# Optimization experiments

Measured on AMD Instinct MI355X. Metric: run time of the kernel, lower is better.

## Reference

```python
import jax, jax.numpy as jnp
import numpy as np

DIM, HEADS, DHEAD = 256, 8, 64
HID = HEADS * DHEAD


def _elu1(x):
    # F.elu(x) + 1 == exp(x) for x<0, x+1 for x>=0
    return jnp.where(x > 0, x + 1.0, jnp.exp(x))


def setup_inputs() -> dict:
    key = jax.random.key(0)
    ks = jax.random.split(key, 6)
    B, H, W = 8, 64, 64
    x = jax.random.normal(ks[0], (B, DIM, H, W), dtype=jnp.float32)
    contact_map = jax.random.uniform(ks[1], (B, 1, H, W), dtype=jnp.float32)
    s_qkv = 1.0 / np.sqrt(DIM)
    Wqkv = jax.random.normal(ks[2], (3 * HID, DIM), dtype=jnp.float32) * s_qkv
    s_out = 1.0 / np.sqrt(HID)
    Wout = jax.random.normal(ks[3], (DIM, HID), dtype=jnp.float32) * s_out
    bout = jax.random.normal(ks[4], (DIM,), dtype=jnp.float32) * 0.01
    contact_scale = jnp.float32(0.1)
    return {"x": x, "contact_map": contact_map, "Wqkv": Wqkv,
            "Wout": Wout, "bout": bout, "contact_scale": contact_scale}


def reference(x, contact_map, Wqkv, Wout, bout, contact_scale):
    b, c, h, w = x.shape
    n = h * w
    xf = x.reshape(b, c, n)                                  # b c n
    qkv = jnp.einsum('oc,bcn->bon', Wqkv, xf)                # b (3*H*D) n
    qkv = qkv.reshape(b, 3, HEADS, DHEAD, n)                 # qkv-major channel order
    q = _elu1(qkv[:, 0])                                     # b h d n
    k = _elu1(qkv[:, 1])
    v = qkv[:, 2]
    cm = contact_map.reshape(b, 1, 1, n)                     # b 1 1 n
    k = k * (1.0 + contact_scale * cm)
    kv = jnp.einsum('bhdn,bhen->bhde', k, v)                 # b h d e
    ksum = k.sum(axis=-1)                                    # b h d
    z = 1.0 / (jnp.einsum('bhdn,bhd->bhn', q, ksum) + 1e-6)  # b h n
    out = jnp.einsum('bhde,bhdn->bhne', kv, q) * z[..., None]  # b h n e
    out = out.transpose(0, 1, 3, 2).reshape(b, HID, n)       # b (h d) n
    y = jnp.einsum('oc,bcn->bon', Wout, out) + bout[None, :, None]
    return y.reshape(b, -1, h, w)
```

## Files before the change

kernel.cpp:

```cpp
#include <hip/hip_runtime.h>
#include <stdint.h>


#define NPIX 4096
#define HIDC 512
#define DIMC 256
#define BATCH 8

typedef __attribute__((ext_vector_type(8))) short bf16x8;
typedef __attribute__((ext_vector_type(4))) float f32x4;
typedef __attribute__((ext_vector_type(16))) float f32x16;

__device__ __forceinline__ float bf2f(unsigned short h) {
    unsigned int u = ((unsigned int)h) << 16; float f;
    __builtin_memcpy(&f, &u, 4); return f;
}
__device__ __forceinline__ unsigned short f2bf(float f) {
    unsigned int u; __builtin_memcpy(&u, &f, 4);
    u += 0x7fffu + ((u >> 16) & 1u);
    return (unsigned short)(u >> 16);
}
__device__ __forceinline__ float elu1(float x) {
    return x > 0.f ? x + 1.f : __expf(x);
}

__global__ __launch_bounds__(256) void k_convW(
    const float* __restrict__ Wqkv, const float* __restrict__ Wout,
    unsigned short* __restrict__ Wb, unsigned short* __restrict__ Wob)
{
    int i4 = (blockIdx.x * 256 + threadIdx.x) * 4;
    const int NW1 = 1536 * 256;
    float4 v; unsigned short* dst;
    if (i4 < NW1) { v = *(const float4*)&Wqkv[i4]; dst = Wb + i4; }
    else { int j = i4 - NW1; v = *(const float4*)&Wout[j]; dst = Wob + j; }
    ushort4 o; o.x = f2bf(v.x); o.y = f2bf(v.y); o.z = f2bf(v.z); o.w = f2bf(v.w);
    *(ushort4*)dst = o;
}

__global__ __launch_bounds__(256) void k_tx(
    const float* __restrict__ x, unsigned short* __restrict__ xT)
{
    __shared__ float tile[32][33];
    const int n0 = blockIdx.x * 32, c0 = blockIdx.y * 32, b = blockIdx.z;
    const int t = threadIdx.x;
    const int r = t >> 3, c4 = (t & 7) * 4;
    float4 v = *(const float4*)&x[((size_t)b * DIMC + c0 + r) * NPIX + n0 + c4];
    tile[r][c4 + 0] = v.x; tile[r][c4 + 1] = v.y;
    tile[r][c4 + 2] = v.z; tile[r][c4 + 3] = v.w;
    __syncthreads();
    ushort4 o;
    unsigned short* op = (unsigned short*)&o;
#pragma unroll
    for (int i = 0; i < 4; i++) op[i] = f2bf(tile[c4 + i][r]);
    *(ushort4*)&xT[((size_t)b * NPIX + n0 + r) * DIMC + c0 + c4] = o;
}

#define LS1 40
__global__ __launch_bounds__(256) void k_qkv(
    const unsigned short* __restrict__ xT,
    const unsigned short* __restrict__ Wb,
    const float* __restrict__ cmp,
    const float* __restrict__ csp,
    unsigned short* __restrict__ qT,
    unsigned short* __restrict__ kb,
    unsigned short* __restrict__ vb)
{
    const int b  = blockIdx.z;
    const int m0 = blockIdx.x * 128;
    const int n0 = blockIdx.y * 128;
    const int t = threadIdx.x;
    const int wave = t >> 6, lane = t & 63;
    const int wm = wave >> 1, wn = wave & 1;
    const int l31 = lane & 31, lhi = lane >> 5;
    const int sect = n0 >> 9;

    __shared__ unsigned short As[128 * LS1];
    __shared__ unsigned short Bs[128 * LS1];

    const unsigned short* Ag = xT + ((size_t)b * NPIX + m0) * DIMC;
    const unsigned short* Bg = Wb + (size_t)n0 * DIMC;

    const unsigned short* mArr = (sect == 0) ? As : Bs;
    const unsigned short* nArr = (sect == 0) ? Bs : As;

    f32x16 acc[2][2];
#pragma unroll
    for (int i = 0; i < 2; i++)
#pragma unroll
        for (int j = 0; j < 2; j++)
#pragma unroll
            for (int r = 0; r < 16; r++) acc[i][j][r] = 0.f;

    const int srow = t >> 2, sc8 = (t & 3) * 8;
    for (int k0 = 0; k0 < DIMC; k0 += 32) {
        *(uint4*)&As[srow * LS1 + sc8] =
            *(const uint4*)&Ag[(size_t)srow * DIMC + k0 + sc8];
        *(uint4*)&As[(srow + 64) * LS1 + sc8] =
            *(const uint4*)&Ag[(size_t)(srow + 64) * DIMC + k0 + sc8];
        *(uint4*)&Bs[srow * LS1 + sc8] =
            *(const uint4*)&Bg[(size_t)srow * DIMC + k0 + sc8];
        *(uint4*)&Bs[(srow + 64) * LS1 + sc8] =
            *(const uint4*)&Bg[(size_t)(srow + 64) * DIMC + k0 + sc8];
        __syncthreads();
#pragma unroll
        for (int ks = 0; ks < 2; ks++) {
            bf16x8 af[2], bfg[2];
#pragma unroll
            for (int fm = 0; fm < 2; fm++)
                af[fm] = *(const bf16x8*)&mArr[(wm * 64 + fm * 32 + l31) * LS1 + ks * 16 + lhi * 8];
#pragma unroll
            for (int fn = 0; fn < 2; fn++)
                bfg[fn] = *(const bf16x8*)&nArr[(wn * 64 + fn * 32 + l31) * LS1 + ks * 16 + lhi * 8];
#pragma unroll
            for (int fm = 0; fm < 2; fm++)
#pragma unroll
                for (int fn = 0; fn < 2; fn++)
                    acc[fm][fn] = __builtin_amdgcn_mfma_f32_32x32x16_bf16(
                        af[fm], bfg[fn], acc[fm][fn], 0, 0, 0);
        }
        __syncthreads();
    }

    const float cs = *csp;
    if (sect == 0) {
#pragma unroll
        for (int fm = 0; fm < 2; fm++) {
            const int pbase = m0 + wm * 64 + fm * 32;
#pragma unroll
            for (int fn = 0; fn < 2; fn++) {
                const int o = n0 + wn * 64 + fn * 32 + l31;
#pragma unroll
                for (int r = 0; r < 16; r++) {
                    int prow = pbase + (r & 3) + 8 * (r >> 2) + 4 * lhi;
                    qT[((size_t)b * NPIX + prow) * HIDC + o] = f2bf(elu1(acc[fm][fn][r]));
                }
            }
        }
    } else {
        unsigned short* dstb = (sect == 1) ? kb : vb;
#pragma unroll
        for (int fm = 0; fm < 2; fm++) {
            const int obase = (n0 & 511) + wm * 64 + fm * 32;
#pragma unroll
            for (int fn = 0; fn < 2; fn++) {
                const int pixel = m0 + wn * 64 + fn * 32 + l31;
                float g = 1.f;
                if (sect == 1) g = 1.f + cs * cmp[(size_t)b * NPIX + pixel];
#pragma unroll
                for (int r = 0; r < 16; r++) {
                    int orow = obase + (r & 3) + 8 * (r >> 2) + 4 * lhi;
                    float val = acc[fm][fn][r];
                    if (sect == 1) val = elu1(val) * g;
                    dstb[((size_t)b * HIDC + orow) * NPIX + pixel] = f2bf(val);
                }
            }
        }
    }
}

#define LS2 40
__global__ __launch_bounds__(256) void k_kv(
    const unsigned short* __restrict__ kb, const unsigned short* __restrict__ vb,
    float* __restrict__ kv, float* __restrict__ ksum)
{
    const int bh = blockIdx.y, nc = blockIdx.x;
    const int t = threadIdx.x, wave = t >> 6, lane = t & 63;
    const int lrow = lane & 15, quad = lane >> 4;

    __shared__ unsigned short ks[64 * LS2];
    __shared__ unsigned short vs[64 * LS2];

    const size_t base = (size_t)bh * 64 * NPIX;
    f32x4 acc[4];
#pragma unroll
    for (int i = 0; i < 4; i++) acc[i] = (f32x4){0.f, 0.f, 0.f, 0.f};
    float ksacc = 0.f;

    const int row = t >> 2, c8 = (t & 3) * 8;

    for (int step = 0; step < 16; step++) {
        const int ncol = nc * 512 + step * 32;
        uint4 kq = *(const uint4*)&kb[base + (size_t)row * NPIX + ncol + c8];
        *(uint4*)&ks[row * LS2 + c8] = kq;
        *(uint4*)&vs[row * LS2 + c8] = *(const uint4*)&vb[base + (size_t)row * NPIX + ncol + c8];
        const unsigned short* kp = (const unsigned short*)&kq;
#pragma unroll
        for (int j = 0; j < 8; j++) ksacc += bf2f(kp[j]);
        __syncthreads();
        bf16x8 bfv = *(const bf16x8*)&vs[(wave * 16 + lrow) * LS2 + quad * 8];
#pragma unroll
        for (int mt = 0; mt < 4; mt++) {
            bf16x8 af = *(const bf16x8*)&ks[(mt * 16 + lrow) * LS2 + quad * 8];
            acc[mt] = __builtin_amdgcn_mfma_f32_16x16x32_bf16(af, bfv, acc[mt], 0, 0, 0);
        }
        __syncthreads();
    }

    float* kvb = kv + (size_t)bh * 4096;
#pragma unroll
    for (int mt = 0; mt < 4; mt++)
#pragma unroll
        for (int r = 0; r < 4; r++)
            atomicAdd(&kvb[(mt * 16 + quad * 4 + r) * 64 + wave * 16 + lrow], acc[mt][r]);
    atomicAdd(&ksum[bh * 64 + row], ksacc);
}

#define LS3 72
__global__ __launch_bounds__(256) void k_out(
    const unsigned short* __restrict__ qT,
    const float* __restrict__ kv, const float* __restrict__ ksum,
    unsigned short* __restrict__ outT)
{
    const int bh = blockIdx.y, p0 = blockIdx.x * 128;
    const int b = bh >> 3, h = bh & 7;
    const int t = threadIdx.x, wave = t >> 6, lane = t & 63;
    const int l31 = lane & 31, lhi = lane >> 5;

    __shared__ unsigned short Aq[128 * LS3];
    __shared__ unsigned short Bv[96 * LS3];

    const unsigned short* qg = qT + ((size_t)b * NPIX + p0) * HIDC + h * 64;
#pragma unroll
    for (int i = 0; i < 4; i++) {
        int idx = t + i * 256;
        int row = idx >> 3, c8 = (idx & 7) * 8;
        *(uint4*)&Aq[row * LS3 + c8] = *(const uint4*)&qg[(size_t)row * HIDC + c8];
    }
    const float* kvg = kv + (size_t)bh * 4096;
#pragma unroll
    for (int i = 0; i < 16; i++) {
        int idx = t + i * 256;
        int d = idx >> 6, e = idx & 63;
        Bv[e * LS3 + d] = f2bf(kvg[idx]);
    }
    if (t < 64) {
        float ksv = ksum[bh * 64 + t];
        unsigned short hi = f2bf(ksv);
        Bv[64 * LS3 + t] = hi;
        Bv[65 * LS3 + t] = f2bf(ksv - bf2f(hi));
    }
    for (int i = t; i < 30 * 64; i += 256)
        Bv[(66 + (i >> 6)) * LS3 + (i & 63)] = 0;
    __syncthreads();

    f32x16 acc[3];
#pragma unroll
    for (int j = 0; j < 3; j++)
#pragma unroll
        for (int r = 0; r < 16; r++) acc[j][r] = 0.f;

#pragma unroll
    for (int ksub = 0; ksub < 4; ksub++) {
        const int koff = ksub * 16 + lhi * 8;
        bf16x8 af = *(const bf16x8*)&Aq[(wave * 32 + l31) * LS3 + koff];
#pragma unroll
        for (int nf = 0; nf < 3; nf++) {
            bf16x8 bfg = *(const bf16x8*)&Bv[(nf * 32 + l31) * LS3 + koff];
            acc[nf] = __builtin_amdgcn_mfma_f32_32x32x16_bf16(af, bfg, acc[nf], 0, 0, 0);
        }
    }

    unsigned short* og = outT + ((size_t)b * NPIX + p0 + wave * 32) * HIDC + h * 64;
#pragma unroll
    for (int r = 0; r < 16; r++) {
        float hi = __shfl(acc[2][r], lane & 32);
        float lo = __shfl(acc[2][r], (lane & 32) | 1);
        float z = 1.f / (hi + lo + 1e-6f);
        int prow = (r & 3) + 8 * (r >> 2) + 4 * lhi;
#pragma unroll
        for (int nf = 0; nf < 2; nf++)
            og[(size_t)prow * HIDC + nf * 32 + l31] = f2bf(acc[nf][r] * z);
    }
}

__global__ __launch_bounds__(256) void k_y(
    const unsigned short* __restrict__ outT,
    const unsigned short* __restrict__ Wob,
    const float* __restrict__ bout,
    float* __restrict__ y)
{
    const int b  = blockIdx.z;
    const int m0 = blockIdx.x * 128;
    const int n0 = blockIdx.y * 128;
    const int t = threadIdx.x;
    const int wave = t >> 6, lane = t & 63;
    const int wm = wave >> 1, wn = wave & 1;
    const int lrow = lane & 15, quad = lane >> 4;

    __shared__ unsigned short As[128 * LS1];
    __shared__ unsigned short Bs[128 * LS1];

    const unsigned short* Ag = outT + ((size_t)b * NPIX + m0) * HIDC;
    const unsigned short* Bg = Wob + (size_t)n0 * HIDC;

    f32x4 acc[4][4];
#pragma unroll
    for (int i = 0; i < 4; i++)
#pragma unroll
        for (int j = 0; j < 4; j++) acc[i][j] = (f32x4){0.f, 0.f, 0.f, 0.f};

    const int srow = t >> 2, sc8 = (t & 3) * 8;
    for (int k0 = 0; k0 < HIDC; k0 += 32) {
        *(uint4*)&As[srow * LS1 + sc8] =
            *(const uint4*)&Ag[(size_t)srow * HIDC + k0 + sc8];
        *(uint4*)&As[(srow + 64) * LS1 + sc8] =
            *(const uint4*)&Ag[(size_t)(srow + 64) * HIDC + k0 + sc8];
        *(uint4*)&Bs[srow * LS1 + sc8] =
            *(const uint4*)&Bg[(size_t)srow * HIDC + k0 + sc8];
        *(uint4*)&Bs[(srow + 64) * LS1 + sc8] =
            *(const uint4*)&Bg[(size_t)(srow + 64) * HIDC + k0 + sc8];
        __syncthreads();
        bf16x8 af[4], bfr[4];
#pragma unroll
        for (int mt = 0; mt < 4; mt++)
            af[mt] = *(const bf16x8*)&As[(wm * 64 + mt * 16 + lrow) * LS1 + quad * 8];
#pragma unroll
        for (int nt = 0; nt < 4; nt++)
            bfr[nt] = *(const bf16x8*)&Bs[(wn * 64 + nt * 16 + lrow) * LS1 + quad * 8];
#pragma unroll
        for (int mt = 0; mt < 4; mt++)
#pragma unroll
            for (int nt = 0; nt < 4; nt++)
                acc[mt][nt] = __builtin_amdgcn_mfma_f32_16x16x32_bf16(
                    af[mt], bfr[nt], acc[mt][nt], 0, 0, 0);
        __syncthreads();
    }

#pragma unroll
    for (int mt = 0; mt < 4; mt++) {
        const int pixel0 = m0 + wm * 64 + mt * 16 + quad * 4;
#pragma unroll
        for (int nt = 0; nt < 4; nt++) {
            const int o = n0 + wn * 64 + nt * 16 + lrow;
            const float bias = bout[o];
            f32x4 a = acc[mt][nt];
            float4 st; st.x = a[0] + bias; st.y = a[1] + bias;
            st.z = a[2] + bias; st.w = a[3] + bias;
            *(float4*)&y[((size_t)b * DIMC + o) * NPIX + pixel0] = st;
        }
    }
}

extern "C" void kernel_launch(void* const* d_in, const int* in_sizes, int n_in,
                              void* d_out, int out_size, void* d_ws, size_t ws_size,
                              hipStream_t stream) {
    (void)in_sizes; (void)n_in; (void)out_size; (void)ws_size;
    const float* x    = (const float*)d_in[0];
    const float* cm   = (const float*)d_in[1];
    const float* Wqkv = (const float*)d_in[2];
    const float* Wout = (const float*)d_in[3];
    const float* bout = (const float*)d_in[4];
    const float* csp  = (const float*)d_in[5];
    float* y = (float*)d_out;

    const size_t qn = (size_t)BATCH * HIDC * NPIX;
    char* ws = (char*)d_ws;
    unsigned short* qT   = (unsigned short*)ws;                 ws += qn * 2;
    unsigned short* kb   = (unsigned short*)ws;                 ws += qn * 2;
    unsigned short* vb   = (unsigned short*)ws;                 ws += qn * 2;
    unsigned short* outT = (unsigned short*)ws;                 ws += qn * 2;
    unsigned short* xT   = outT;
    float* kvp   = (float*)ws;                                  ws += (size_t)64 * 64 * 64 * 4;
    float* ksump = (float*)ws;                                  ws += (size_t)64 * 64 * 4;
    unsigned short* Wb  = (unsigned short*)ws;                  ws += (size_t)1536 * 256 * 2;
    unsigned short* Wob = (unsigned short*)ws;

    hipMemsetAsync(kvp, 0, ((size_t)64 * 64 * 64 + 64 * 64) * sizeof(float), stream);
    k_convW<<<512, 256, 0, stream>>>(Wqkv, Wout, Wb, Wob);
    k_tx  <<<dim3(128, 8, 8), 256, 0, stream>>>(x, xT);
    k_qkv <<<dim3(32, 12, 8), 256, 0, stream>>>(xT, Wb, cm, csp, qT, kb, vb);
    k_kv  <<<dim3(8, 64),     256, 0, stream>>>(kb, vb, kvp, ksump);
    k_out <<<dim3(32, 64),    256, 0, stream>>>(qT, kvp, ksump, outT);
    k_y   <<<dim3(32, 2, 8),  256, 0, stream>>>(outT, Wob, bout, y);
}
```

Measured before the change: 214.8 us.

## Use direct global-to-LDS loads with XOR-swizzled tiles and BK=64 in GEMMs

The QKV and output-projection GEMM kernels now stage tiles with global_load_lds 16-byte transfers straight into LDS instead of going through registers. To avoid bank conflicts without padding, the LDS layout is XOR-swizzled, and the K step is doubled to 64, which halves the number of barriers. This cuts register pressure and VGPR round-trips, but LDS use per block roughly doubles and the swizzle indexing must match exactly between the store and read sides.

```diff
diff --git a/kernel.cpp b/kernel.cpp
--- a/kernel.cpp
+++ b/kernel.cpp
@@ -22,6 +22,11 @@
 }
 __device__ __forceinline__ float elu1(float x) {
     return x > 0.f ? x + 1.f : __expf(x);
+}
+__device__ __forceinline__ void gl16(const unsigned short* g, unsigned short* l) {
+    __builtin_amdgcn_global_load_lds(
+        (__attribute__((address_space(1))) const void*)g,
+        (__attribute__((address_space(3))) void*)l, 16, 0, 0);
 }
 
 __global__ __launch_bounds__(256) void k_convW(
@@ -55,7 +60,6 @@
     *(ushort4*)&xT[((size_t)b * NPIX + n0 + r) * DIMC + c0 + c4] = o;
 }
 
-#define LS1 40
 __global__ __launch_bounds__(256) void k_qkv(
     const unsigned short* __restrict__ xT,
     const unsigned short* __restrict__ Wb,
@@ -74,8 +78,8 @@
     const int l31 = lane & 31, lhi = lane >> 5;
     const int sect = n0 >> 9;
 
-    __shared__ unsigned short As[128 * LS1];
-    __shared__ unsigned short Bs[128 * LS1];
+    __shared__ unsigned short As[128 * 64];
+    __shared__ unsigned short Bs[128 * 64];
 
     const unsigned short* Ag = xT + ((size_t)b * NPIX + m0) * DIMC;
     const unsigned short* Bg = Wb + (size_t)n0 * DIMC;
@@ -91,26 +95,28 @@
 #pragma unroll
             for (int r = 0; r < 16; r++) acc[i][j][r] = 0.f;
 
-    const int srow = t >> 2, sc8 = (t & 3) * 8;
-    for (int k0 = 0; k0 < DIMC; k0 += 32) {
-        *(uint4*)&As[srow * LS1 + sc8] =
-            *(const uint4*)&Ag[(size_t)srow * DIMC + k0 + sc8];
-        *(uint4*)&As[(srow + 64) * LS1 + sc8] =
-            *(const uint4*)&Ag[(size_t)(srow + 64) * DIMC + k0 + sc8];
-        *(uint4*)&Bs[srow * LS1 + sc8] =
-            *(const uint4*)&Bg[(size_t)srow * DIMC + k0 + sc8];
-        *(uint4*)&Bs[(srow + 64) * LS1 + sc8] =
-            *(const uint4*)&Bg[(size_t)(srow + 64) * DIMC + k0 + sc8];
-        __syncthreads();
-#pragma unroll
-        for (int ks = 0; ks < 2; ks++) {
+    const int r8  = lane >> 3;
+    const int jg8 = (((lane & 7) ^ r8) & 7) * 8;
+    const int xsw = (l31 & 7);
+
+    for (int k0 = 0; k0 < DIMC; k0 += 64) {
+#pragma unroll
+        for (int i = 0; i < 4; i++) {
+            const int rowg = wave * 32 + i * 8;
+            gl16(&Ag[(size_t)(rowg + r8) * DIMC + k0 + jg8], &As[rowg * 64]);
+            gl16(&Bg[(size_t)(rowg + r8) * DIMC + k0 + jg8], &Bs[rowg * 64]);
+        }
+        __syncthreads();
+#pragma unroll
+        for (int ks = 0; ks < 4; ks++) {
+            const int coff = ((ks * 2 + lhi) ^ xsw) * 8;
             bf16x8 af[2], bfg[2];
 #pragma unroll
             for (int fm = 0; fm < 2; fm++)
-                af[fm] = *(const bf16x8*)&mArr[(wm * 64 + fm * 32 + l31) * LS1 + ks * 16 + lhi * 8];
+                af[fm] = *(const bf16x8*)&mArr[(wm * 64 + fm * 32 + l31) * 64 + coff];
 #pragma unroll
             for (int fn = 0; fn < 2; fn++)
-                bfg[fn] = *(const bf16x8*)&nArr[(wn * 64 + fn * 32 + l31) * LS1 + ks * 16 + lhi * 8];
+                bfg[fn] = *(const bf16x8*)&nArr[(wn * 64 + fn * 32 + l31) * 64 + coff];
 #pragma unroll
             for (int fm = 0; fm < 2; fm++)
 #pragma unroll
@@ -287,8 +293,8 @@
     const int wm = wave >> 1, wn = wave & 1;
     const int lrow = lane & 15, quad = lane >> 4;
 
-    __shared__ unsigned short As[128 * LS1];
-    __shared__ unsigned short Bs[128 * LS1];
+    __shared__ unsigned short As[128 * 64];
+    __shared__ unsigned short Bs[128 * 64];
 
     const unsigned short* Ag = outT + ((size_t)b * NPIX + m0) * HIDC;
     const unsigned short* Bg = Wob + (size_t)n0 * HIDC;
@@ -299,30 +305,38 @@
 #pragma unroll
         for (int j = 0; j < 4; j++) acc[i][j] = (f32x4){0.f, 0.f, 0.f, 0.f};
 
-    const int srow = t >> 2, sc8 = (t & 3) * 8;
-    for (int k0 = 0; k0 < HIDC; k0 += 32) {
-        *(uint4*)&As[srow * LS1 + sc8] =
-            *(const uint4*)&Ag[(size_t)srow * HIDC + k0 + sc8];
-        *(uint4*)&As[(srow + 64) * LS1 + sc8] =
-            *(const uint4*)&Ag[(size_t)(srow + 64) * HIDC + k0 + sc8];
-        *(uint4*)&Bs[srow * LS1 + sc8] =
-            *(const uint4*)&Bg[(size_t)srow * HIDC + k0 + sc8];
-        *(uint4*)&Bs[(srow + 64) * LS1 + sc8] =
-            *(const uint4*)&Bg[(size_t)(srow + 64) * HIDC + k0 + sc8];
-        __syncthreads();
-        bf16x8 af[4], bfr[4];
-#pragma unroll
-        for (int mt = 0; mt < 4; mt++)
-            af[mt] = *(const bf16x8*)&As[(wm * 64 + mt * 16 + lrow) * LS1 + quad * 8];
-#pragma unroll
-        for (int nt = 0; nt < 4; nt++)
-            bfr[nt] = *(const bf16x8*)&Bs[(wn * 64 + nt * 16 + lrow) * LS1 + quad * 8];
-#pragma unroll
-        for (int mt = 0; mt < 4; mt++)
-#pragma unroll
-            for (int nt = 0; nt < 4; nt++)
-                acc[mt][nt] = __builtin_amdgcn_mfma_f32_16x16x32_bf16(
-                    af[mt], bfr[nt], acc[mt][nt], 0, 0, 0);
+    const int r8  = lane >> 3;
+    const int jg8 = (((lane & 7) ^ r8) & 7) * 8;
+    const int xswA = (lrow & 7);
+
+    for (int k0 = 0; k0 < HIDC; k0 += 64) {
+#pragma unroll
+        for (int i = 0; i < 4; i++) {
+            const int rowg = wave * 32 + i * 8;
+            gl16(&Ag[(size_t)(rowg + r8) * HIDC + k0 + jg8], &As[rowg * 64]);
+            gl16(&Bg[(size_t)(rowg + r8) * HIDC + k0 + jg8], &Bs[rowg * 64]);
+        }
+        __syncthreads();
+#pragma unroll
+        for (int ksb = 0; ksb < 2; ksb++) {
+            bf16x8 af[4], bfr[4];
+#pragma unroll
+            for (int mt = 0; mt < 4; mt++) {
+                const int row = wm * 64 + mt * 16 + lrow;
+                af[mt] = *(const bf16x8*)&As[row * 64 + (((ksb * 4 + quad) ^ xswA)) * 8];
+            }
+#pragma unroll
+            for (int nt = 0; nt < 4; nt++) {
+                const int row = wn * 64 + nt * 16 + lrow;
+                bfr[nt] = *(const bf16x8*)&Bs[row * 64 + (((ksb * 4 + quad) ^ xswA)) * 8];
+            }
+#pragma unroll
+            for (int mt = 0; mt < 4; mt++)
+#pragma unroll
+                for (int nt = 0; nt < 4; nt++)
+                    acc[mt][nt] = __builtin_amdgcn_mfma_f32_16x16x32_bf16(
+                        af[mt], bfr[nt], acc[mt][nt], 0, 0, 0);
+        }
         __syncthreads();
     }
 
```

Result: faster. 206.3 us (-4.0%).
